# Kernel optimization log

Hardware: AMD Instinct MI355X
Metric: run time of the kernel (lower is better)

The kernel has to match this reference:

```python
import jax, jax.numpy as jnp
import numpy as np

NUM_FEATURES = 512
NUM_HEADS = 8
DIM_PER_HEAD = NUM_FEATURES // NUM_HEADS


def setup_inputs() -> dict:
    key = jax.random.key(0)
    ks = jax.random.split(key, 9)
    B, C, H, W = 8, NUM_FEATURES, 32, 32
    # xavier_uniform bound for 1x1 conv: sqrt(6/(fan_in+fan_out)) = sqrt(6/(2C))
    bound = float(np.sqrt(6.0 / (2.0 * C)))
    # conv bias default init: U(-1/sqrt(fan_in), 1/sqrt(fan_in))
    bbound = float(1.0 / np.sqrt(C))
    return {
        "query": jax.random.normal(ks[0], (B, C, H, W), jnp.float32),
        "key": jax.random.normal(ks[1], (B, C, H, W), jnp.float32),
        "value": jax.random.normal(ks[2], (B, C, H, W), jnp.float32),
        "wq": jax.random.uniform(ks[3], (C, C), jnp.float32, -bound, bound),
        "bq": jax.random.uniform(ks[4], (C,), jnp.float32, -bbound, bbound),
        "wk": jax.random.uniform(ks[5], (C, C), jnp.float32, -bound, bound),
        "bk": jax.random.uniform(ks[6], (C,), jnp.float32, -bbound, bbound),
        "wv": jax.random.uniform(ks[7], (C, C), jnp.float32, -bound, bound),
        "bv": jax.random.uniform(ks[8], (C,), jnp.float32, -bbound, bbound),
    }


def _proj(x, w, b):
    # 1x1 conv == per-pixel linear over channels. x: [B,C,H,W], w: [Cout,Cin]
    return jnp.einsum('oi,bihw->bohw', w, x) + b[None, :, None, None]


def _split_heads(x, nh, d):
    B, C, H, W = x.shape
    # view (B, nh, d, H*W) then permute -> (B, nh, S, d)
    return x.reshape(B, nh, d, H * W).transpose(0, 1, 3, 2)


def reference(query, key, value, wq, bq, wk, bk, wv, bv):
    B, C, H, W = query.shape
    nh, d = NUM_HEADS, DIM_PER_HEAD
    q = _split_heads(_proj(query, wq, bq), nh, d)   # [B,nh,S,d]
    k = _split_heads(_proj(key, wk, bk), nh, d)
    v = _split_heads(_proj(value, wv, bv), nh, d)
    scores = jnp.einsum('bhsd,bhtd->bhst', q, k) / jnp.sqrt(jnp.float32(d))
    attn = jax.nn.softmax(scores, axis=-1)          # [B,nh,S,S]
    out = jnp.einsum('bhst,bhtd->bhsd', attn, v)    # [B,nh,S,d]
    # combine_heads (faithful to torch): permute to (B,S,nh,d), flat reshape
    out = out.transpose(0, 2, 1, 3)                 # [B,S,nh,d]
    return out.reshape(B, C, H, W)
```

## Files before the change

### kernel.cpp

```cpp
#include <hip/hip_runtime.h>
#include <hip/hip_bf16.h>
#include <stdint.h>


typedef __attribute__((ext_vector_type(4))) float f32x4;
typedef __attribute__((ext_vector_type(8))) short short8;
typedef __attribute__((ext_vector_type(4))) unsigned int u32x4;

#define GLB_AS(p) ((const __attribute__((address_space(1))) void*)(p))
#define LDS_AS(p) ((__attribute__((address_space(3))) void*)(p))

__device__ __forceinline__ unsigned short f2b(float f) {
  unsigned int x = __builtin_bit_cast(unsigned int, f);
  x = (x + 0x7FFFu + ((x >> 16) & 1u)) >> 16;
  return (unsigned short)x;
}

__device__ __forceinline__ float exp2_hw(float x) {
  float r;
  asm("v_exp_f32 %0, %1" : "=v"(r) : "v"(x));
  return r;
}

__device__ __forceinline__ unsigned int cvtpk(float lo, float hi) {
  unsigned int r;
  asm("v_cvt_pk_bf16_f32 %0, %1, %2" : "=v"(r) : "v"(lo), "v"(hi));
  return r;
}

__device__ __forceinline__ f32x4 mfma16(short8 a, short8 b, f32x4 c) {
  return __builtin_amdgcn_mfma_f32_16x16x32_bf16(a, b, c, 0, 0, 0);
}

__global__ __launch_bounds__(256) void transpose_cast3(const float* __restrict__ Xq,
                                                       const float* __restrict__ Xk,
                                                       const float* __restrict__ Xv,
                                                       unsigned short* __restrict__ Xt) {
  __shared__ float t[64][65];
  const int which = blockIdx.z >> 3, bb = blockIdx.z & 7;
  const float* X = (which == 0) ? Xq : ((which == 1) ? Xk : Xv);
  const int s0 = blockIdx.x * 64, c0 = blockIdx.y * 64;
  const float* Xb = X + (long)bb * 512 * 1024;
  const int tid = threadIdx.x;
  const int col4 = (tid & 15) * 4;
  const int r0 = tid >> 4;
#pragma unroll
  for (int it = 0; it < 4; ++it) {
    int r = r0 + it * 16;
    const float4 v = *(const float4*)&Xb[(long)(c0 + r) * 1024 + s0 + col4];
    t[r][col4 + 0] = v.x; t[r][col4 + 1] = v.y; t[r][col4 + 2] = v.z; t[r][col4 + 3] = v.w;
  }
  __syncthreads();
  const int s = tid >> 2;
  const int cp = (tid & 3) * 16;
  unsigned int u[8];
#pragma unroll
  for (int i = 0; i < 8; ++i) {
    unsigned int lo = f2b(t[cp + 2 * i][s]);
    unsigned int hi = f2b(t[cp + 2 * i + 1][s]);
    u[i] = lo | (hi << 16);
  }
  unsigned short* dst = Xt + (long)which * 8 * 1024 * 512 +
                        ((long)bb * 1024 + s0 + s) * 512 + c0 + cp;
  ((uint4*)dst)[0] = make_uint4(u[0], u[1], u[2], u[3]);
  ((uint4*)dst)[1] = make_uint4(u[4], u[5], u[6], u[7]);
}

__global__ __launch_bounds__(256) void cast_w3(const float* __restrict__ wq,
                                               const float* __restrict__ wk,
                                               const float* __restrict__ wv,
                                               unsigned short* __restrict__ O) {
  const int y = blockIdx.y;
  const float* W = (y == 0) ? wq : ((y == 1) ? wk : wv);
  int i = blockIdx.x * 256 + threadIdx.x;
  float4 v = ((const float4*)W)[i];
  uint2 u;
  u.x = (unsigned)f2b(v.x) | ((unsigned)f2b(v.y) << 16);
  u.y = (unsigned)f2b(v.z) | ((unsigned)f2b(v.w) << 16);
  ((uint2*)(O + (long)y * 262144))[i] = u;
}

__global__ __launch_bounds__(256, 2) void gemm_proj(
    const unsigned short* __restrict__ XT, const unsigned short* __restrict__ W3,
    unsigned short* __restrict__ QKV, const float* __restrict__ bq,
    const float* __restrict__ bk, const float* __restrict__ bv) {
  __shared__ __align__(16) unsigned short lA[128 * 64];
  __shared__ __align__(16) unsigned short lB[128 * 64];
  const long SC = 1024L * 512;
  const int bid = blockIdx.x;
  const int kind = bid >> 8;
  const int rr = bid & 255;
  const int batch = rr >> 5, tile = rr & 31;
  const unsigned short *Ab, *Bb;
  unsigned short* Cb;
  const float* bias;
  int m0, n0, N, biasN;
  float scale = 1.0f;
  if (kind < 2) {
    m0 = (tile >> 2) * 128; n0 = (tile & 3) * 128; N = 512; biasN = 1;
    Ab = XT + ((long)kind * 8 + batch) * SC;
    Bb = W3 + (long)kind * 262144;
    Cb = QKV + ((long)kind * 8 + batch) * SC;
    bias = kind ? bk : bq;
    if (kind == 0) scale = 0.18033688011112042f;
  } else {
    m0 = (tile >> 3) * 128; n0 = (tile & 7) * 128; N = 1024; biasN = 0;
    Ab = W3 + 2 * 262144;
    Bb = XT + (16L + batch) * SC;
    Cb = QKV + (16L + batch) * SC;
    bias = bv;
  }
  const int tid = threadIdx.x, lane = tid & 63, wid = tid >> 6;
  const int wr = wid >> 1, wc = wid & 1;
  const int lm = lane & 15, lg = lane >> 4;
  f32x4 acc[4][4] = {};
  for (int k0 = 0; k0 < 512; k0 += 64) {
#pragma unroll
    for (int ch = wid; ch < 16; ch += 4) {
      int e = ch * 512 + lane * 8;
      int r = e >> 6, cc = e & 63;
      __builtin_amdgcn_global_load_lds(GLB_AS(Ab + (long)(m0 + r) * 512 + k0 + cc),
                                       LDS_AS(lA + ch * 512), 16, 0, 0);
      __builtin_amdgcn_global_load_lds(GLB_AS(Bb + (long)(n0 + r) * 512 + k0 + cc),
                                       LDS_AS(lB + ch * 512), 16, 0, 0);
    }
    __syncthreads();
#pragma unroll
    for (int kk = 0; kk < 2; ++kk) {
      short8 af[4], bf[4];
#pragma unroll
      for (int i = 0; i < 4; ++i)
        af[i] = *(const short8*)&lA[(wr * 64 + i * 16 + lm) * 64 + kk * 32 + 8 * lg];
#pragma unroll
      for (int j = 0; j < 4; ++j)
        bf[j] = *(const short8*)&lB[(wc * 64 + j * 16 + lm) * 64 + kk * 32 + 8 * lg];
#pragma unroll
      for (int i = 0; i < 4; ++i)
#pragma unroll
        for (int j = 0; j < 4; ++j)
          acc[i][j] = mfma16(af[i], bf[j], acc[i][j]);
    }
    __syncthreads();
  }
#pragma unroll
  for (int i = 0; i < 4; ++i)
#pragma unroll
    for (int j = 0; j < 4; ++j)
#pragma unroll
      for (int r = 0; r < 4; ++r) {
        int m = m0 + wr * 64 + i * 16 + lg * 4 + r;
        int n = n0 + wc * 64 + j * 16 + lm;
        float bvv = biasN ? bias[n] : bias[m];
        Cb[(long)m * N + n] = f2b((acc[i][j][r] + bvv) * scale);
      }
}

__global__ __launch_bounds__(256, 2) void attn(
    const unsigned short* __restrict__ Qt, const unsigned short* __restrict__ Kt,
    const unsigned short* __restrict__ V, float* __restrict__ Out) {
  __shared__ __align__(16) unsigned short lK[3][64 * 64];
  __shared__ __align__(16) unsigned short lV[3][64 * 64];
  const int flat = blockIdx.x;
  const int xcd = flat & 7, j = flat >> 3;
  const int pair = xcd * 8 + (j >> 3);
  const int st = j & 7;
  const int b = pair >> 3, h = pair & 7;
  const int tid = threadIdx.x, lane = tid & 63, w = tid >> 6;
  const int lm = lane & 15, lg = lane >> 4;
  const int s0 = st * 128 + w * 32;
  const unsigned short* Qb = Qt + ((long)b * 1024 + s0) * 512 + h * 64;
  const unsigned short* Kb = Kt + (long)b * 1024 * 512 + h * 64;
  const unsigned short* Vb = V + ((long)b * 512 + h * 64) * 1024;

  const int srow = (w << 1) * 8 + (lane >> 3);
  const int scol = ((lane & 7) ^ (lane >> 3)) * 8;
  auto stage = [&](int buf, int t0) {
#pragma unroll
    for (int jj = 0; jj < 2; ++jj) {
      int ch = (w << 1) + jj;
      int row = srow + jj * 8;
      __builtin_amdgcn_global_load_lds(GLB_AS(Kb + (long)(t0 + row) * 512 + scol),
                                       LDS_AS(&lK[buf][ch * 512]), 16, 0, 0);
      __builtin_amdgcn_global_load_lds(GLB_AS(Vb + (long)row * 1024 + t0 + scol),
                                       LDS_AS(&lV[buf][ch * 512]), 16, 0, 0);
    }
  };

  short8 qf[2][2];
#pragma unroll
  for (int si = 0; si < 2; ++si)
#pragma unroll
    for (int kk = 0; kk < 2; ++kk)
      qf[si][kk] = *(const short8*)&Qb[(si * 16 + lm) * 512 + kk * 32 + 8 * lg];

  f32x4 o[2][4] = {};
  float lsum[2] = {};

  stage(0, 0);
  stage(1, 64);
  asm volatile("s_waitcnt vmcnt(4) lgkmcnt(0)" ::: "memory");
  __builtin_amdgcn_s_barrier();
  __builtin_amdgcn_sched_barrier(0);

#pragma unroll 1
  for (int t = 0; t < 16; ++t) {
    const int cur = t % 3;
    if (t < 14) stage((t + 2) % 3, (t + 2) * 64);
    f32x4 s[2][4] = {};
    __builtin_amdgcn_s_setprio(1);
#pragma unroll
    for (int tj = 0; tj < 4; ++tj) {
      short8 kf0 = *(const short8*)&lK[cur][(tj * 16 + lm) * 64 + 8 * (lg ^ (lm & 7))];
      short8 kf1 = *(const short8*)&lK[cur][(tj * 16 + lm) * 64 + 8 * ((lg + 4) ^ (lm & 7))];
#pragma unroll
      for (int si = 0; si < 2; ++si) {
        s[si][tj] = mfma16(kf0, qf[si][0], s[si][tj]);
        s[si][tj] = mfma16(kf1, qf[si][1], s[si][tj]);
      }
    }
    __builtin_amdgcn_s_setprio(0);
#pragma unroll
    for (int si = 0; si < 2; ++si)
#pragma unroll
      for (int tj = 0; tj < 4; ++tj)
#pragma unroll
        for (int r = 0; r < 4; ++r) {
          float p = exp2_hw(s[si][tj][r]);
          s[si][tj][r] = p;
          lsum[si] += p;
        }
#pragma unroll
    for (int tk = 0; tk < 2; ++tk) {
      short8 pa[2];
#pragma unroll
      for (int si = 0; si < 2; ++si) {
        unsigned int X01 = cvtpk(s[si][2 * tk][0], s[si][2 * tk][1]);
        unsigned int X23 = cvtpk(s[si][2 * tk][2], s[si][2 * tk][3]);
        unsigned int Y01 = cvtpk(s[si][2 * tk + 1][0], s[si][2 * tk + 1][1]);
        unsigned int Y23 = cvtpk(s[si][2 * tk + 1][2], s[si][2 * tk + 1][3]);
        asm("v_permlane32_swap_b32 %0, %1" : "+v"(X01), "+v"(Y01));
        asm("v_permlane32_swap_b32 %0, %1" : "+v"(X23), "+v"(Y23));
        asm("v_permlane16_swap_b32 %0, %1" : "+v"(X01), "+v"(Y01));
        asm("v_permlane16_swap_b32 %0, %1" : "+v"(X23), "+v"(Y23));
        u32x4 pw;
        pw[0] = X01;
        pw[1] = X23;
        pw[2] = Y01;
        pw[3] = Y23;
        pa[si] = __builtin_bit_cast(short8, pw);
      }
      __builtin_amdgcn_s_setprio(1);
#pragma unroll
      for (int dj = 0; dj < 4; ++dj) {
        short8 vf = *(const short8*)&lV[cur][(dj * 16 + lm) * 64 + 8 * ((tk * 4 + lg) ^ (lm & 7))];
        o[0][dj] = mfma16(pa[0], vf, o[0][dj]);
        o[1][dj] = mfma16(pa[1], vf, o[1][dj]);
      }
      __builtin_amdgcn_s_setprio(0);
    }
    if (t < 14) {
      asm volatile("s_waitcnt vmcnt(4) lgkmcnt(0)" ::: "memory");
      __builtin_amdgcn_s_barrier();
      __builtin_amdgcn_sched_barrier(0);
    } else if (t == 14) {
      asm volatile("s_waitcnt vmcnt(0) lgkmcnt(0)" ::: "memory");
      __builtin_amdgcn_s_barrier();
      __builtin_amdgcn_sched_barrier(0);
    }
  }

  float inv[2][4];
#pragma unroll
  for (int si = 0; si < 2; ++si) {
    float rs = lsum[si];
    rs += __shfl_xor(rs, 16);
    rs += __shfl_xor(rs, 32);
#pragma unroll
    for (int r = 0; r < 4; ++r)
      inv[si][r] = 1.0f / __shfl(rs, lg * 4 + r);
  }
#pragma unroll
  for (int si = 0; si < 2; ++si)
#pragma unroll
    for (int dj = 0; dj < 4; ++dj)
#pragma unroll
      for (int r = 0; r < 4; ++r) {
        int srow2 = s0 + si * 16 + lg * 4 + r;
        Out[((long)b * 1024 + srow2) * 512 + h * 64 + dj * 16 + lm] = o[si][dj][r] * inv[si][r];
      }
}

extern "C" void kernel_launch(void* const* d_in, const int* in_sizes, int n_in,
                              void* d_out, int out_size, void* d_ws, size_t ws_size,
                              hipStream_t stream) {
  const float* query = (const float*)d_in[0];
  const float* key   = (const float*)d_in[1];
  const float* value = (const float*)d_in[2];
  const float* wq = (const float*)d_in[3];
  const float* bq = (const float*)d_in[4];
  const float* wk = (const float*)d_in[5];
  const float* bk = (const float*)d_in[6];
  const float* wv = (const float*)d_in[7];
  const float* bv = (const float*)d_in[8];

  unsigned short* ws = (unsigned short*)d_ws;
  const long SC = 1024L * 512;
  unsigned short* XT  = ws;
  unsigned short* W3  = XT + 24 * SC;
  unsigned short* QKV = W3 + 3 * 262144;
  unsigned short* QT  = QKV;
  unsigned short* KTm = QKV + 8 * SC;
  unsigned short* VVm = QKV + 16 * SC;

  transpose_cast3<<<dim3(16, 8, 24), 256, 0, stream>>>(query, key, value, XT);
  cast_w3<<<dim3(256, 3), 256, 0, stream>>>(wq, wk, wv, W3);
  gemm_proj<<<768, 256, 0, stream>>>(XT, W3, QKV, bq, bk, bv);
  attn<<<512, 256, 0, stream>>>(QT, KTm, VVm, (float*)d_out);
}
```

Before: 69.02 us.

## Fuse weight cast into transpose kernel; attention uses 128-wide KV tiles double-buffered

```diff
diff --git a/kernel.cpp b/kernel.cpp
--- a/kernel.cpp
+++ b/kernel.cpp
@@ -32,16 +32,35 @@
   return __builtin_amdgcn_mfma_f32_16x16x32_bf16(a, b, c, 0, 0, 0);
 }
 
-__global__ __launch_bounds__(256) void transpose_cast3(const float* __restrict__ Xq,
-                                                       const float* __restrict__ Xk,
-                                                       const float* __restrict__ Xv,
-                                                       unsigned short* __restrict__ Xt) {
+__global__ __launch_bounds__(256) void prep_all(const float* __restrict__ Xq,
+                                                const float* __restrict__ Xk,
+                                                const float* __restrict__ Xv,
+                                                const float* __restrict__ wq,
+                                                const float* __restrict__ wk,
+                                                const float* __restrict__ wv,
+                                                unsigned short* __restrict__ Xt,
+                                                unsigned short* __restrict__ WO) {
   __shared__ float t[64][65];
+  const int tid = threadIdx.x;
+  if (blockIdx.z == 24) {
+    const int bid = blockIdx.y * 16 + blockIdx.x;
+#pragma unroll
+    for (int k = 0; k < 6; ++k) {
+      int i = bid * 1536 + k * 256 + tid;
+      int which = i >> 16, off = i & 65535;
+      const float* W = (which == 0) ? wq : ((which == 1) ? wk : wv);
+      float4 v = ((const float4*)W)[off];
+      uint2 u;
+      u.x = (unsigned)f2b(v.x) | ((unsigned)f2b(v.y) << 16);
+      u.y = (unsigned)f2b(v.z) | ((unsigned)f2b(v.w) << 16);
+      ((uint2*)(WO + (long)which * 262144))[off] = u;
+    }
+    return;
+  }
   const int which = blockIdx.z >> 3, bb = blockIdx.z & 7;
   const float* X = (which == 0) ? Xq : ((which == 1) ? Xk : Xv);
   const int s0 = blockIdx.x * 64, c0 = blockIdx.y * 64;
   const float* Xb = X + (long)bb * 512 * 1024;
-  const int tid = threadIdx.x;
   const int col4 = (tid & 15) * 4;
   const int r0 = tid >> 4;
 #pragma unroll
@@ -64,20 +83,6 @@
                         ((long)bb * 1024 + s0 + s) * 512 + c0 + cp;
   ((uint4*)dst)[0] = make_uint4(u[0], u[1], u[2], u[3]);
   ((uint4*)dst)[1] = make_uint4(u[4], u[5], u[6], u[7]);
-}
-
-__global__ __launch_bounds__(256) void cast_w3(const float* __restrict__ wq,
-                                               const float* __restrict__ wk,
-                                               const float* __restrict__ wv,
-                                               unsigned short* __restrict__ O) {
-  const int y = blockIdx.y;
-  const float* W = (y == 0) ? wq : ((y == 1) ? wk : wv);
-  int i = blockIdx.x * 256 + threadIdx.x;
-  float4 v = ((const float4*)W)[i];
-  uint2 u;
-  u.x = (unsigned)f2b(v.x) | ((unsigned)f2b(v.y) << 16);
-  u.y = (unsigned)f2b(v.z) | ((unsigned)f2b(v.w) << 16);
-  ((uint2*)(O + (long)y * 262144))[i] = u;
 }
 
 __global__ __launch_bounds__(256, 2) void gemm_proj(
@@ -158,8 +163,8 @@
 __global__ __launch_bounds__(256, 2) void attn(
     const unsigned short* __restrict__ Qt, const unsigned short* __restrict__ Kt,
     const unsigned short* __restrict__ V, float* __restrict__ Out) {
-  __shared__ __align__(16) unsigned short lK[3][64 * 64];
-  __shared__ __align__(16) unsigned short lV[3][64 * 64];
+  __shared__ __align__(16) unsigned short lK[2][128 * 64];
+  __shared__ __align__(16) unsigned short lV[2][64 * 128];
   const int flat = blockIdx.x;
   const int xcd = flat & 7, j = flat >> 3;
   const int pair = xcd * 8 + (j >> 3);
@@ -172,16 +177,17 @@
   const unsigned short* Kb = Kt + (long)b * 1024 * 512 + h * 64;
   const unsigned short* Vb = V + ((long)b * 512 + h * 64) * 1024;
 
-  const int srow = (w << 1) * 8 + (lane >> 3);
-  const int scol = ((lane & 7) ^ (lane >> 3)) * 8;
+  const int kscol = ((lane & 7) ^ (lane >> 3)) * 8;
   auto stage = [&](int buf, int t0) {
 #pragma unroll
-    for (int jj = 0; jj < 2; ++jj) {
-      int ch = (w << 1) + jj;
-      int row = srow + jj * 8;
-      __builtin_amdgcn_global_load_lds(GLB_AS(Kb + (long)(t0 + row) * 512 + scol),
+    for (int jj = 0; jj < 4; ++jj) {
+      int ch = w * 4 + jj;
+      int krow = ch * 8 + (lane >> 3);
+      __builtin_amdgcn_global_load_lds(GLB_AS(Kb + (long)(t0 + krow) * 512 + kscol),
                                        LDS_AS(&lK[buf][ch * 512]), 16, 0, 0);
-      __builtin_amdgcn_global_load_lds(GLB_AS(Vb + (long)row * 1024 + t0 + scol),
+      int vrow = ch * 4 + (lane >> 4);
+      int vcb = (lane & 15) ^ (vrow & 15);
+      __builtin_amdgcn_global_load_lds(GLB_AS(Vb + (long)vrow * 1024 + t0 + vcb * 8),
                                        LDS_AS(&lV[buf][ch * 512]), 16, 0, 0);
     }
   };
@@ -197,19 +203,16 @@
   float lsum[2] = {};
 
   stage(0, 0);
-  stage(1, 64);
-  asm volatile("s_waitcnt vmcnt(4) lgkmcnt(0)" ::: "memory");
-  __builtin_amdgcn_s_barrier();
-  __builtin_amdgcn_sched_barrier(0);
+  __syncthreads();
 
 #pragma unroll 1
-  for (int t = 0; t < 16; ++t) {
-    const int cur = t % 3;
-    if (t < 14) stage((t + 2) % 3, (t + 2) * 64);
-    f32x4 s[2][4] = {};
+  for (int t = 0; t < 8; ++t) {
+    const int cur = t & 1;
+    if (t < 7) stage(cur ^ 1, (t + 1) * 128);
+    f32x4 s[2][8] = {};
     __builtin_amdgcn_s_setprio(1);
 #pragma unroll
-    for (int tj = 0; tj < 4; ++tj) {
+    for (int tj = 0; tj < 8; ++tj) {
       short8 kf0 = *(const short8*)&lK[cur][(tj * 16 + lm) * 64 + 8 * (lg ^ (lm & 7))];
       short8 kf1 = *(const short8*)&lK[cur][(tj * 16 + lm) * 64 + 8 * ((lg + 4) ^ (lm & 7))];
 #pragma unroll
@@ -222,7 +225,7 @@
 #pragma unroll
     for (int si = 0; si < 2; ++si)
 #pragma unroll
-      for (int tj = 0; tj < 4; ++tj)
+      for (int tj = 0; tj < 8; ++tj)
 #pragma unroll
         for (int r = 0; r < 4; ++r) {
           float p = exp2_hw(s[si][tj][r]);
@@ -230,7 +233,7 @@
           lsum[si] += p;
         }
 #pragma unroll
-    for (int tk = 0; tk < 2; ++tk) {
+    for (int tk = 0; tk < 4; ++tk) {
       short8 pa[2];
 #pragma unroll
       for (int si = 0; si < 2; ++si) {
@@ -252,21 +255,13 @@
       __builtin_amdgcn_s_setprio(1);
 #pragma unroll
       for (int dj = 0; dj < 4; ++dj) {
-        short8 vf = *(const short8*)&lV[cur][(dj * 16 + lm) * 64 + 8 * ((tk * 4 + lg) ^ (lm & 7))];
+        short8 vf = *(const short8*)&lV[cur][(dj * 16 + lm) * 128 + 8 * ((tk * 4 + lg) ^ lm)];
         o[0][dj] = mfma16(pa[0], vf, o[0][dj]);
         o[1][dj] = mfma16(pa[1], vf, o[1][dj]);
       }
       __builtin_amdgcn_s_setprio(0);
     }
-    if (t < 14) {
-      asm volatile("s_waitcnt vmcnt(4) lgkmcnt(0)" ::: "memory");
-      __builtin_amdgcn_s_barrier();
-      __builtin_amdgcn_sched_barrier(0);
-    } else if (t == 14) {
-      asm volatile("s_waitcnt vmcnt(0) lgkmcnt(0)" ::: "memory");
-      __builtin_amdgcn_s_barrier();
-      __builtin_amdgcn_sched_barrier(0);
-    }
+    __syncthreads();
   }
 
   float inv[2][4];
@@ -312,8 +307,7 @@
   unsigned short* KTm = QKV + 8 * SC;
   unsigned short* VVm = QKV + 16 * SC;
 
-  transpose_cast3<<<dim3(16, 8, 24), 256, 0, stream>>>(query, key, value, XT);
-  cast_w3<<<dim3(256, 3), 256, 0, stream>>>(wq, wk, wv, W3);
+  prep_all<<<dim3(16, 8, 25), 256, 0, stream>>>(query, key, value, wq, wk, wv, XT, W3);
   gemm_proj<<<768, 256, 0, stream>>>(XT, W3, QKV, bq, bk, bv);
   attn<<<512, 256, 0, stream>>>(QT, KTm, VVm, (float*)d_out);
 }
```

Result: faster. 65.18 us (-5.6%).
